# Optimization experiments

Measured on AMD Instinct MI355X. Metric: run time of the kernel, lower is better.

## Reference

```python
import math
import jax, jax.numpy as jnp
import numpy as np

B, S, H = 2, 2048, 1024
NH = 16
HD = H // NH  # 64
THETA = 10000.0


def _rope_cache(seq_len, head_dim, theta):
    inv_freq = 1.0 / (theta ** (jnp.arange(0, head_dim, 2, dtype=jnp.float32) / head_dim))
    pos = jnp.arange(seq_len, dtype=jnp.float32)
    freqs = jnp.outer(pos, inv_freq)           # (S, HD/2)
    emb = jnp.concatenate([freqs, freqs], -1)  # (S, HD)
    return jnp.cos(emb), jnp.sin(emb)


def _apply_rotary(x, cos, sin):
    # x: (B, NH, S, HD); cos/sin: (S, HD) broadcast over B, NH
    d = x.shape[-1] // 2
    x1, x2 = x[..., :d], x[..., d:]
    rotated = jnp.concatenate([-x2, x1], -1)
    return x * cos + rotated * sin


def setup_inputs() -> dict:
    key = jax.random.key(0)
    ks = jax.random.split(key, 5)
    scale = 1.0 / math.sqrt(H)
    return {
        'x': jax.random.normal(ks[0], (B, S, H), jnp.float32),
        'Wq': jax.random.normal(ks[1], (H, H), jnp.float32) * scale,
        'Wk': jax.random.normal(ks[2], (H, H), jnp.float32) * scale,
        'Wv': jax.random.normal(ks[3], (H, H), jnp.float32) * scale,
        'Wo': jax.random.normal(ks[4], (H, H), jnp.float32) * scale,
    }


def reference(x, Wq, Wk, Wv, Wo):
    b, s, h = x.shape
    # projections (nn.Linear: x @ W.T)
    q = (x @ Wq.T).reshape(b, s, NH, HD).transpose(0, 2, 1, 3)
    k = (x @ Wk.T).reshape(b, s, NH, HD).transpose(0, 2, 1, 3)
    v = (x @ Wv.T).reshape(b, s, NH, HD).transpose(0, 2, 1, 3)
    cos, sin = _rope_cache(s, HD, THETA)
    q = _apply_rotary(q, cos, sin)
    k = _apply_rotary(k, cos, sin)
    scale = 1.0 / math.sqrt(HD)
    attn = jnp.einsum('bhqd,bhkd->bhqk', q, k) * scale
    causal = jnp.triu(jnp.ones((s, s), dtype=bool), k=1)
    attn = jnp.where(causal, -jnp.inf, attn)
    attn = jax.nn.softmax(attn, axis=-1)
    out = jnp.einsum('bhqk,bhkd->bhqd', attn, v)
    out = out.transpose(0, 2, 1, 3).reshape(b, s, h)
    return out @ Wo.T
```

## Files before the change

kernel.cpp:

```cpp
#include <hip/hip_runtime.h>

#define B_  2
#define S_  2048
#define H_  1024
#define NH_ 16
#define HD_ 64
#define M_  (B_ * S_)

typedef short  short8  __attribute__((ext_vector_type(8)));
typedef __bf16 bf16x8  __attribute__((ext_vector_type(8)));
typedef float  f32x4   __attribute__((ext_vector_type(4)));

__device__ __forceinline__ ushort f2bf(float f) {
  union { float f; unsigned u; } v; v.f = f;
  unsigned r = v.u + 0x7fffu + ((v.u >> 16) & 1u);
  return (ushort)(r >> 16);
}
__device__ __forceinline__ float bf2f(ushort u) {
  union { unsigned u; float f; } v; v.u = ((unsigned)u) << 16;
  return v.f;
}
__device__ __forceinline__ unsigned cvtpk(float lo, float hi) {
  unsigned r;
  asm("v_cvt_pk_bf16_f32 %0, %1, %2" : "=v"(r) : "v"(lo), "v"(hi));
  return r;
}

__device__ __forceinline__ void gload_lds16(const void* g, void* l) {
  __builtin_amdgcn_global_load_lds(
      (const __attribute__((address_space(1))) void*)g,
      (__attribute__((address_space(3))) void*)l, 16, 0, 0);
}

__device__ __forceinline__ f32x4 mfma_bf16(short8 a, short8 b, f32x4 c) {
  return __builtin_amdgcn_mfma_f32_16x16x32_bf16(
      __builtin_bit_cast(bf16x8, a), __builtin_bit_cast(bf16x8, b), c, 0, 0, 0);
}

__device__ __forceinline__ int swzK(int r, int c) {
  return r * 64 + ((c ^ (r & 7)) << 3);
}
__device__ __forceinline__ int swzV(int r, int c) {
  return r * 128 + ((c ^ (r & 7)) << 3);
}

__device__ __forceinline__ float redmax64(float a) {
  a = fmaxf(a, __shfl_xor(a, 16));
  a = fmaxf(a, __shfl_xor(a, 32));
  return a;
}

__global__ __launch_bounds__(256)
void prep(const float* __restrict__ x, const float* __restrict__ Wq,
          const float* __restrict__ Wk, const float* __restrict__ Wv,
          const float* __restrict__ Wo, ushort* __restrict__ xb,
          ushort* __restrict__ Wqkv, ushort* __restrict__ Wob,
          float* __restrict__ ct, float* __restrict__ st) {
  int bid = blockIdx.x, t = threadIdx.x;
  if (bid < 4096) {
    int i = (bid * 256 + t) * 4;
    float4 v = *(const float4*)&x[i];
    ushort4 o;
    o.x = f2bf(v.x); o.y = f2bf(v.y); o.z = f2bf(v.z); o.w = f2bf(v.w);
    *(ushort4*)&xb[i] = o;
  } else if (bid < 8192) {
    int y = (bid - 4096) >> 10;
    const float* src = (y == 0) ? Wq : (y == 1) ? Wk : (y == 2) ? Wv : Wo;
    ushort* dst = (y == 3) ? Wob : Wqkv + (size_t)y * H_ * H_;
    int i = (((bid - 4096) & 1023) * 256 + t) * 4;
    float4 v = *(const float4*)&src[i];
    ushort4 o;
    o.x = f2bf(v.x); o.y = f2bf(v.y); o.z = f2bf(v.z); o.w = f2bf(v.w);
    *(ushort4*)&dst[i] = o;
  } else {
    int i = (bid - 8192) * 256 + t;
    int pos = i >> 5, d2 = i & 31;
    float invf = powf(10000.0f, -(float)d2 / 32.0f);
    float fr = (float)pos * invf;
    ct[i] = cosf(fr);
    st[i] = sinf(fr);
  }
}

template <int MODE>
__global__ __launch_bounds__(256)
void gemm_bt(const ushort* __restrict__ A, const ushort* __restrict__ Bm,
             void* __restrict__ Cout, int Mdim, int Ndim, int Kdim,
             const float* __restrict__ ct, const float* __restrict__ st,
             ushort* __restrict__ qb, ushort* __restrict__ kb,
             ushort* __restrict__ vt) {
  __shared__ ushort SMEM[128 * 128];
  ushort* As = SMEM;
  ushort* Bs = SMEM + 128 * 64;
  int t = threadIdx.x;
  int w = t >> 6, l = t & 63;
  int m0 = blockIdx.y * 128, n0 = blockIdx.x * 128;
  int wr = (w >> 1) * 64, wc = (w & 1) * 64;
  int lrow = l & 15, g = l >> 4;

  f32x4 acc[4][4];
#pragma unroll
  for (int mi = 0; mi < 4; ++mi)
#pragma unroll
    for (int ni = 0; ni < 4; ++ni) acc[mi][ni] = f32x4{0.f, 0.f, 0.f, 0.f};

  for (int k0 = 0; k0 < Kdim; k0 += 64) {
    __syncthreads();
#pragma unroll
    for (int cc = 0; cc < 4; ++cc) {
      int slot = cc * 256 + t;
      int r = slot >> 3, c = slot & 7;
      int cs = (c ^ (r & 7)) << 3;
      gload_lds16(&A[(size_t)(m0 + r) * Kdim + k0 + cs], &As[slot * 8]);
      gload_lds16(&Bm[(size_t)(n0 + r) * Kdim + k0 + cs], &Bs[slot * 8]);
    }
    __syncthreads();
#pragma unroll
    for (int kk = 0; kk < 2; ++kk) {
      short8 af[4], bfr[4];
#pragma unroll
      for (int i = 0; i < 4; ++i)
        af[i] = *(const short8*)&As[swzK(wr + i * 16 + lrow, kk * 4 + g)];
#pragma unroll
      for (int i = 0; i < 4; ++i)
        bfr[i] = *(const short8*)&Bs[swzK(wc + i * 16 + lrow, kk * 4 + g)];
#pragma unroll
      for (int mi = 0; mi < 4; ++mi)
#pragma unroll
        for (int ni = 0; ni < 4; ++ni)
          acc[mi][ni] = mfma_bf16(af[mi], bfr[ni], acc[mi][ni]);
    }
  }

  if (MODE == 0) {
#pragma unroll
    for (int mi = 0; mi < 4; ++mi)
#pragma unroll
      for (int ni = 0; ni < 4; ++ni)
#pragma unroll
        for (int j = 0; j < 4; ++j) {
          int row = m0 + wr + mi * 16 + g * 4 + j;
          int col = n0 + wc + ni * 16 + lrow;
          ((float*)Cout)[(size_t)row * Ndim + col] = acc[mi][ni][j];
        }
  } else {
    int colbase = n0 + wc;
    int sector = n0 >> 10;
    int h = (colbase & 1023) >> 6;
    if (sector < 2) {
      ushort* dst = (sector == 0) ? qb : kb;
      const float SCq = (sector == 0) ? 0.125f * 1.44269504f : 1.0f;
#pragma unroll
      for (int mi = 0; mi < 4; ++mi)
#pragma unroll
        for (int j = 0; j < 4; ++j) {
          int row = m0 + wr + mi * 16 + g * 4 + j;
          int b = row >> 11, s = row & 2047;
          size_t o = ((size_t)(b * NH_ + h) * S_ + s) * HD_;
          float c0 = ct[s * 32 + lrow],      s0 = st[s * 32 + lrow];
          float c1 = ct[s * 32 + 16 + lrow], s1 = st[s * 32 + 16 + lrow];
          float x1a = acc[mi][0][j], x2a = acc[mi][2][j];
          float x1b = acc[mi][1][j], x2b = acc[mi][3][j];
          dst[o + lrow]      = f2bf((x1a * c0 - x2a * s0) * SCq);
          dst[o + lrow + 32] = f2bf((x2a * c0 + x1a * s0) * SCq);
          dst[o + lrow + 16] = f2bf((x1b * c1 - x2b * s1) * SCq);
          dst[o + lrow + 48] = f2bf((x2b * c1 + x1b * s1) * SCq);
        }
    } else {
      __syncthreads();
#pragma unroll
      for (int mi = 0; mi < 4; ++mi) {
        int s_local = wr + mi * 16 + g * 4;
#pragma unroll
        for (int ni = 0; ni < 4; ++ni) {
          int cl = wc + ni * 16 + lrow;
          uint2 pk;
          pk.x = cvtpk(acc[mi][ni][0], acc[mi][ni][1]);
          pk.y = cvtpk(acc[mi][ni][2], acc[mi][ni][3]);
          int a = cl * 128 + (((s_local >> 3) ^ (cl & 7)) << 3) + (s_local & 7);
          *(uint2*)&SMEM[a] = pk;
        }
      }
      __syncthreads();
      int b = m0 >> 11, s_base = m0 & 2047;
#pragma unroll
      for (int cc = 0; cc < 2; ++cc) {
        int u = cc * 256 + t;
        int cl = u >> 2;
        int sq = (u & 3) * 32;
        int hh = ((n0 + cl) & 1023) >> 6;
        int d  = cl & 63;
        size_t ob = ((size_t)(b * NH_ + hh) * HD_ + d) * S_ + s_base + sq;
#pragma unroll
        for (int i = 0; i < 4; ++i) {
          int sl = sq + i * 8;
          int a = cl * 128 + (((sl >> 3) ^ (cl & 7)) << 3);
          *(short8*)&vt[ob + i * 8] = *(const short8*)&SMEM[a];
        }
      }
    }
  }
}

__global__ __launch_bounds__(512, 4)
void flash_attn(const ushort* __restrict__ qb, const ushort* __restrict__ kb,
                const ushort* __restrict__ vt, ushort* __restrict__ ctx) {
  __shared__ ushort Ks[128 * 64];
  __shared__ ushort Vs[2][64 * 128];
  __shared__ ushort Ps[128 * 64];
  int bh = blockIdx.y;
  int qt = (blockIdx.y & 16) ? (int)blockIdx.x : (15 - (int)blockIdx.x);
  int b = bh >> 4, h = bh & 15;
  int t = threadIdx.x, w = t >> 6, l = t & 63;
  int lrow = l & 15, g = l >> 4;
  int wrow = w * 16;
  const ushort* Q = qb + (size_t)bh * S_ * HD_;
  const ushort* K = kb + (size_t)bh * S_ * HD_;
  const ushort* V = vt + (size_t)bh * HD_ * S_;

  short8 ones;
#pragma unroll
  for (int i = 0; i < 8; ++i) ones[i] = (short)0x3F80;

#pragma unroll
  for (int cc = 0; cc < 2; ++cc) {
    int slot = cc * 512 + t;
    int r = slot >> 3, c = slot & 7;
    int cs = (c ^ (r & 7)) << 3;
    gload_lds16(&K[(size_t)r * 64 + cs], &Ks[slot * 8]);
  }
#pragma unroll
  for (int cc = 0; cc < 2; ++cc) {
    int slot = cc * 512 + t;
    int r = slot >> 4, c = slot & 15;
    int cs = (c ^ (r & 7)) << 3;
    gload_lds16(&V[(size_t)r * S_ + cs], &Vs[0][slot * 8]);
  }
  short8 aq[2];
  {
    int qrow = qt * 128 + wrow + lrow;
#pragma unroll
    for (int ks = 0; ks < 2; ++ks)
      aq[ks] = *(const short8*)&Q[(size_t)qrow * 64 + ks * 32 + g * 8];
  }
  __syncthreads();

  float m_ = -1e30f, ls_ = 0.f;
  f32x4 O[4];
#pragma unroll
  for (int nf = 0; nf < 4; ++nf) O[nf] = f32x4{0.f, 0.f, 0.f, 0.f};

  int nkt = qt + 1;
  for (int kt = 0; kt < nkt; ++kt) {
    const ushort* Vc = Vs[kt & 1];

    f32x4 sc[8];
#pragma unroll
    for (int nf = 0; nf < 8; ++nf) sc[nf] = f32x4{0.f, 0.f, 0.f, 0.f};
    __builtin_amdgcn_s_setprio(1);
#pragma unroll
    for (int ks = 0; ks < 2; ++ks)
#pragma unroll
      for (int nf = 0; nf < 8; ++nf) {
        short8 bk = *(const short8*)&Ks[swzK(nf * 16 + lrow, ks * 4 + g)];
        sc[nf] = mfma_bf16(bk, aq[ks], sc[nf]);
      }
    __builtin_amdgcn_s_setprio(0);

    __syncthreads();

    if (kt + 1 < nkt) {
      int nb = (kt + 1) & 1;
#pragma unroll
      for (int cc = 0; cc < 2; ++cc) {
        int slot = cc * 512 + t;
        int r = slot >> 3, c = slot & 7;
        int cs = (c ^ (r & 7)) << 3;
        gload_lds16(&K[(size_t)((kt + 1) * 128 + r) * 64 + cs], &Ks[slot * 8]);
      }
#pragma unroll
      for (int cc = 0; cc < 2; ++cc) {
        int slot = cc * 512 + t;
        int r = slot >> 4, c = slot & 15;
        int cs = (c ^ (r & 7)) << 3;
        gload_lds16(&V[(size_t)r * S_ + (kt + 1) * 128 + cs], &Vs[nb][slot * 8]);
      }
    }

    int qbase = qt * 128 + wrow;
    if (kt * 128 + 127 > qbase) {
      int qi = qbase + lrow;
#pragma unroll
      for (int nf = 0; nf < 8; ++nf) {
        int kbase = kt * 128 + nf * 16 + g * 4;
#pragma unroll
        for (int j = 0; j < 4; ++j)
          if (kbase + j > qi) sc[nf][j] = -1e30f;
      }
    }

    f32x4 v4 = sc[0];
#pragma unroll
    for (int nf = 1; nf < 8; ++nf)
#pragma unroll
      for (int j = 0; j < 4; ++j) v4[j] = fmaxf(v4[j], sc[nf][j]);
    float mx = redmax64(fmaxf(fmaxf(v4[0], v4[1]), fmaxf(v4[2], v4[3])));

    bool nor = __all(mx <= m_ + 8.f);
    if (!nor) {
      float mnew = fmaxf(m_, mx);
      float al = exp2f(m_ - mnew);
      m_ = mnew;
      ls_ *= al;
#pragma unroll
      for (int nf = 0; nf < 4; ++nf)
#pragma unroll
        for (int j = 0; j < 4; ++j) O[nf][j] *= al;
    }

#pragma unroll
    for (int nf = 0; nf < 8; ++nf)
#pragma unroll
      for (int j = 0; j < 4; ++j) sc[nf][j] = exp2f(sc[nf][j] - m_);

    f32x4 sacc = f32x4{0.f, 0.f, 0.f, 0.f};
#pragma unroll
    for (int half = 0; half < 2; ++half) {
      int prow = wrow + lrow;
#pragma unroll
      for (int nf2 = 0; nf2 < 4; ++nf2) {
        int nf = half * 4 + nf2;
        uint2 pk;
        pk.x = cvtpk(sc[nf][0], sc[nf][1]);
        pk.y = cvtpk(sc[nf][2], sc[nf][3]);
        *(uint2*)&Ps[swzK(prow, nf2 * 2 + (g >> 1)) + (g & 1) * 4] = pk;
      }
      __builtin_amdgcn_s_setprio(1);
#pragma unroll
      for (int ks2 = 0; ks2 < 2; ++ks2) {
        short8 ap = *(const short8*)&Ps[swzK(wrow + lrow, ks2 * 4 + g)];
        sacc = mfma_bf16(ones, ap, sacc);
#pragma unroll
        for (int nf = 0; nf < 4; ++nf) {
          short8 bv = *(const short8*)&Vc[swzV(nf * 16 + lrow, half * 8 + ks2 * 4 + g)];
          O[nf] = mfma_bf16(bv, ap, O[nf]);
        }
      }
      __builtin_amdgcn_s_setprio(0);
    }
    ls_ += sacc[0];

    __syncthreads();
  }

  float inv = 1.f / ls_;
  int srow = qt * 128 + wrow + lrow;
#pragma unroll
  for (int nf = 0; nf < 4; ++nf) {
    uint2 pk;
    pk.x = cvtpk(O[nf][0] * inv, O[nf][1] * inv);
    pk.y = cvtpk(O[nf][2] * inv, O[nf][3] * inv);
    *(uint2*)&ctx[((size_t)b * S_ + srow) * H_ + h * 64 + nf * 16 + g * 4] = pk;
  }
}

extern "C" void kernel_launch(void* const* d_in, const int* in_sizes, int n_in,
                              void* d_out, int out_size, void* d_ws, size_t ws_size,
                              hipStream_t stream) {
  const float* x  = (const float*)d_in[0];
  const float* Wq = (const float*)d_in[1];
  const float* Wk = (const float*)d_in[2];
  const float* Wv = (const float*)d_in[3];
  const float* Wo = (const float*)d_in[4];

  char* ws = (char*)d_ws;
  size_t off = 0;
  ushort* xb   = (ushort*)(ws + off); off += (size_t)M_ * H_ * 2;
  ushort* Wqkv = (ushort*)(ws + off); off += (size_t)3 * H_ * H_ * 2;
  ushort* Wob  = (ushort*)(ws + off); off += (size_t)H_ * H_ * 2;
  float*  ct   = (float*)(ws + off);  off += (size_t)S_ * 32 * 4;
  float*  st   = (float*)(ws + off);  off += (size_t)S_ * 32 * 4;
  ushort* qb   = (ushort*)(ws + off); off += (size_t)M_ * H_ * 2;
  ushort* kb   = (ushort*)(ws + off); off += (size_t)M_ * H_ * 2;
  ushort* vtb  = (ushort*)(ws + off); off += (size_t)M_ * H_ * 2;
  ushort* ctx  = (ushort*)(ws + off); off += (size_t)M_ * H_ * 2;

  prep<<<8448, 256, 0, stream>>>(x, Wq, Wk, Wv, Wo, xb, Wqkv, Wob, ct, st);

  gemm_bt<2><<<dim3(3 * H_ / 128, M_ / 128), 256, 0, stream>>>(
      xb, Wqkv, nullptr, M_, 3 * H_, H_, ct, st, qb, kb, vtb);
  flash_attn<<<dim3(S_ / 128, B_ * NH_), 512, 0, stream>>>(qb, kb, vtb, ctx);
  gemm_bt<0><<<dim3(H_ / 128, M_ / 128), 256, 0, stream>>>(
      ctx, Wob, d_out, M_, H_, H_, nullptr, nullptr, nullptr, nullptr, nullptr);
}
```

Measured before the change: 120.5 us.

## Double-buffer GEMM LDS tiles with K=32 steps and prefetch next tile

The bf16 GEMM main loop now keeps two 128x32 A and B buffers in shared memory and issues the global-to-LDS loads for the next K slice before computing on the current one, leaving one barrier per iteration instead of two. The K step shrinks from 64 to 32 and the XOR swizzle is dropped in favour of a plain row-major layout. The aim is to overlap memory latency with MFMA work. The cost is twice as many loop iterations, and unswizzled LDS reads with a 64-byte row stride may cause bank conflicts.

```diff
diff --git a/kernel.cpp b/kernel.cpp
--- a/kernel.cpp
+++ b/kernel.cpp
@@ -90,13 +90,16 @@
              ushort* __restrict__ qb, ushort* __restrict__ kb,
              ushort* __restrict__ vt) {
   __shared__ ushort SMEM[128 * 128];
-  ushort* As = SMEM;
-  ushort* Bs = SMEM + 128 * 64;
+  ushort* As0 = SMEM;
+  ushort* As1 = SMEM + 4096;
+  ushort* Bs0 = SMEM + 8192;
+  ushort* Bs1 = SMEM + 12288;
   int t = threadIdx.x;
   int w = t >> 6, l = t & 63;
   int m0 = blockIdx.y * 128, n0 = blockIdx.x * 128;
   int wr = (w >> 1) * 64, wc = (w & 1) * 64;
-  int lrow = l & 15, g = l >> 4;
+  int lrow = l & 15, g = l >> 4, lk8 = g * 8;
+  int arow = t >> 2, acol = (t & 3) * 8;
 
   f32x4 acc[4][4];
 #pragma unroll
@@ -104,32 +107,45 @@
 #pragma unroll
     for (int ni = 0; ni < 4; ++ni) acc[mi][ni] = f32x4{0.f, 0.f, 0.f, 0.f};
 
-  for (int k0 = 0; k0 < Kdim; k0 += 64) {
+#pragma unroll
+  for (int c = 0; c < 2; ++c) {
+    gload_lds16(&A[(size_t)(m0 + arow + c * 64) * Kdim + acol],
+                &As0[(c * 256 + w * 64) * 8]);
+    gload_lds16(&Bm[(size_t)(n0 + arow + c * 64) * Kdim + acol],
+                &Bs0[(c * 256 + w * 64) * 8]);
+  }
+  __syncthreads();
+
+  int nk = Kdim >> 5;
+  for (int ki = 0; ki < nk; ++ki) {
+    int cur = ki & 1;
+    if (ki + 1 < nk) {
+      int k0 = (ki + 1) << 5;
+      ushort* An = cur ? As0 : As1;
+      ushort* Bn = cur ? Bs0 : Bs1;
+#pragma unroll
+      for (int c = 0; c < 2; ++c) {
+        gload_lds16(&A[(size_t)(m0 + arow + c * 64) * Kdim + k0 + acol],
+                    &An[(c * 256 + w * 64) * 8]);
+        gload_lds16(&Bm[(size_t)(n0 + arow + c * 64) * Kdim + k0 + acol],
+                    &Bn[(c * 256 + w * 64) * 8]);
+      }
+    }
+    const ushort* Ac = cur ? As1 : As0;
+    const ushort* Bc = cur ? Bs1 : Bs0;
+    short8 af[4], bfr[4];
+#pragma unroll
+    for (int i = 0; i < 4; ++i)
+      af[i] = *(const short8*)&Ac[(wr + i * 16 + lrow) * 32 + lk8];
+#pragma unroll
+    for (int i = 0; i < 4; ++i)
+      bfr[i] = *(const short8*)&Bc[(wc + i * 16 + lrow) * 32 + lk8];
+#pragma unroll
+    for (int mi = 0; mi < 4; ++mi)
+#pragma unroll
+      for (int ni = 0; ni < 4; ++ni)
+        acc[mi][ni] = mfma_bf16(af[mi], bfr[ni], acc[mi][ni]);
     __syncthreads();
-#pragma unroll
-    for (int cc = 0; cc < 4; ++cc) {
-      int slot = cc * 256 + t;
-      int r = slot >> 3, c = slot & 7;
-      int cs = (c ^ (r & 7)) << 3;
-      gload_lds16(&A[(size_t)(m0 + r) * Kdim + k0 + cs], &As[slot * 8]);
-      gload_lds16(&Bm[(size_t)(n0 + r) * Kdim + k0 + cs], &Bs[slot * 8]);
-    }
-    __syncthreads();
-#pragma unroll
-    for (int kk = 0; kk < 2; ++kk) {
-      short8 af[4], bfr[4];
-#pragma unroll
-      for (int i = 0; i < 4; ++i)
-        af[i] = *(const short8*)&As[swzK(wr + i * 16 + lrow, kk * 4 + g)];
-#pragma unroll
-      for (int i = 0; i < 4; ++i)
-        bfr[i] = *(const short8*)&Bs[swzK(wc + i * 16 + lrow, kk * 4 + g)];
-#pragma unroll
-      for (int mi = 0; mi < 4; ++mi)
-#pragma unroll
-        for (int ni = 0; ni < 4; ++ni)
-          acc[mi][ni] = mfma_bf16(af[mi], bfr[ni], acc[mi][ni]);
-    }
   }
 
   if (MODE == 0) {
```

Result: faster. 110.4 us (-8.4%).
